# Kernel optimization log

Measured on AMD Instinct MI355X. Metric: run time of the kernel, lower is better.

The kernel has to match this reference:

```python
import jax, jax.numpy as jnp
import numpy as np

BN_EPS = 1e-5
LEAKY_SLOPE = 0.2

B, C, N, K, OUT = 8, 64, 4096, 32, 64


def setup_inputs() -> dict:
    key = jax.random.key(0)
    ks = jax.random.split(key, 8)
    return {
        "Graph_index": jax.random.randint(ks[0], (B, N, K), 0, N),
        "x": jax.random.normal(ks[1], (B, C, N), dtype=jnp.float32),
        "feature": jax.random.normal(ks[2], (B, OUT, N, K), dtype=jnp.float32),
        "W": jax.random.normal(ks[3], (OUT, 2 * C), dtype=jnp.float32) * 0.1,
        "gamma": jax.random.uniform(ks[4], (OUT,), dtype=jnp.float32) + 0.5,
        "beta": jax.random.normal(ks[5], (OUT,), dtype=jnp.float32) * 0.1,
        "bn_mean": jax.random.normal(ks[6], (OUT,), dtype=jnp.float32) * 0.1,
        "bn_var": jax.random.uniform(ks[7], (OUT,), dtype=jnp.float32) + 0.5,
    }


def reference(Graph_index, x, feature, W, gamma, beta, bn_mean, bn_var):
    b, c, n = x.shape
    k = Graph_index.shape[-1]
    # torch does x.view(B,N,C): a raw memory reinterpret, not a transpose
    xv = x.reshape(b, n, c)                                  # [B,N,C]
    feat = jnp.transpose(feature, (0, 2, 3, 1))              # [B,N,K,out]
    # index_points: gather K neighbors per point
    nb = jax.vmap(lambda xb, ib: xb[ib])(xv, Graph_index)    # [B,N,K,C]
    centre = xv[:, :, None, :]                               # [B,N,1,C]
    delta_f = jnp.concatenate([centre - nb, nb], axis=3)     # [B,N,K,2C]
    # 1x1 conv over channels == matmul
    e = jnp.einsum("bnkc,oc->bnko", delta_f, W)              # [B,N,K,out]
    # BatchNorm2d (eval-mode affine with running stats)
    inv = gamma * jax.lax.rsqrt(bn_var + BN_EPS)
    e = e * inv + (beta - bn_mean * inv)
    e = jnp.where(e >= 0, e, LEAKY_SLOPE * e)                # LeakyReLU(0.2)
    attention = jax.nn.softmax(e, axis=2)                    # softmax over K
    graph_feature = jnp.sum(attention * feat, axis=2)        # [B,N,out]
    return jnp.transpose(graph_feature, (0, 2, 1))           # [B,out,N]
```

## Files before the change

kernel.cpp:

```cpp
#include <hip/hip_runtime.h>


constexpr int B_ = 8, C_ = 64, N_ = 4096, K_ = 32, O_ = 64;
typedef float v4 __attribute__((ext_vector_type(4)));

__global__ __launch_bounds__(256) void gat_pre(
    const float* __restrict__ x, const float* __restrict__ W,
    const float* __restrict__ gamma, const float* __restrict__ beta,
    const float* __restrict__ bn_mean, const float* __restrict__ bn_var,
    float* __restrict__ T, float* __restrict__ U)
{
    __shared__ float xsT[64][68];
    __shared__ float wt1[64][68];
    __shared__ float wtd[64][68];

    const int blk = blockIdx.x;
    const int b = blk & 7;
    const int n_base = (blk >> 3) << 6;
    const int t = threadIdx.x;

    const float* xb = x + ((size_t)b * N_ + n_base) * C_;
    #pragma unroll
    for (int r = 0; r < 4; ++r) {
        const int e0 = r * 1024 + t * 4;
        const v4 v = __builtin_nontemporal_load(reinterpret_cast<const v4*>(xb + e0));
        xsT[(e0 + 0) & 63][(e0 + 0) >> 6] = v.x;
        xsT[(e0 + 1) & 63][(e0 + 1) >> 6] = v.y;
        xsT[(e0 + 2) & 63][(e0 + 2) >> 6] = v.z;
        xsT[(e0 + 3) & 63][(e0 + 3) >> 6] = v.w;
    }
    #pragma unroll
    for (int i = 0; i < 16; ++i) {
        const int idx = i * 256 + t;
        const int o = idx >> 6, c = idx & 63;
        const float w1 = W[o * 128 + c];
        const float w2 = W[o * 128 + 64 + c];
        wt1[c][o] = w1;
        wtd[c][o] = w2 - w1;
    }
    __syncthreads();

    const int o0 = (t & 15) * 4;
    const int n0 = (t >> 4) * 4;
    float accT[4][4] = {};
    float accU[4][4] = {};
    #pragma unroll 4
    for (int c = 0; c < 64; ++c) {
        const v4 xn = *reinterpret_cast<const v4*>(&xsT[c][n0]);
        const v4 w1 = *reinterpret_cast<const v4*>(&wt1[c][o0]);
        const v4 wd = *reinterpret_cast<const v4*>(&wtd[c][o0]);
        const float xa[4] = {xn.x, xn.y, xn.z, xn.w};
        const float wa[4] = {w1.x, w1.y, w1.z, w1.w};
        const float da[4] = {wd.x, wd.y, wd.z, wd.w};
        #pragma unroll
        for (int i = 0; i < 4; ++i)
            #pragma unroll
            for (int j = 0; j < 4; ++j) {
                accT[i][j] = fmaf(xa[i], wa[j], accT[i][j]);
                accU[i][j] = fmaf(xa[i], da[j], accU[i][j]);
            }
    }

    float inv[4], bias[4];
    #pragma unroll
    for (int j = 0; j < 4; ++j) {
        const int o = o0 + j;
        const float iv = gamma[o] * rsqrtf(bn_var[o] + 1e-5f);
        inv[j] = iv;
        bias[j] = beta[o] - bn_mean[o] * iv;
    }
    #pragma unroll
    for (int i = 0; i < 4; ++i) {
        const int n = n_base + n0 + i;
        float tvv[4], uvv[4];
        #pragma unroll
        for (int j = 0; j < 4; ++j) {
            tvv[j] = fmaf(accT[i][j], inv[j], bias[j]);
            uvv[j] = accU[i][j] * inv[j];
        }
        float* tp = T + ((size_t)b * N_ + n) * O_ + o0;
        float* up = U + ((size_t)b * N_ + n) * O_ + o0;
        *reinterpret_cast<v4*>(tp) = (v4){tvv[0], tvv[1], tvv[2], tvv[3]};
        *reinterpret_cast<v4*>(up) = (v4){uvv[0], uvv[1], uvv[2], uvv[3]};
    }
}

__global__ __launch_bounds__(256) void gat_main(
    const int* __restrict__ gi, const float* __restrict__ feat,
    const float* __restrict__ T, const float* __restrict__ U,
    float* __restrict__ out)
{
    __shared__ float tmp[64][17];
    const int blk = blockIdx.x;
    const int b = blk & 7;
    const int n_base = (blk >> 3) * 16;
    const int t = threadIdx.x;
    const int w = t >> 6;
    const int lane = t & 63;

    const float* Ub = U + (size_t)b * N_ * O_ + lane;

    #pragma unroll 1
    for (int r = 0; r < 4; ++r) {
        const int n = n_base + w * 4 + r;
        int vi = 0;
        if (lane < 32) vi = __builtin_nontemporal_load(&gi[((size_t)b * N_ + n) * K_ + lane]);
        const float tv = __builtin_nontemporal_load(&T[((size_t)b * N_ + n) * O_ + lane]);

        const v4* fp = reinterpret_cast<const v4*>(feat + (((size_t)b * O_ + lane) * N_ + n) * K_);
        v4 f[8];
        #pragma unroll
        for (int k4 = 0; k4 < 8; ++k4) f[k4] = fp[k4];

        float u[32];
        #pragma unroll
        for (int k = 0; k < 32; ++k) {
            const int m = __shfl(vi, k, 64);
            u[k] = Ub[(size_t)m * O_];
        }

        float emax = -3.0e38f;
        #pragma unroll
        for (int k = 0; k < 32; ++k) {
            float ev = tv + u[k];
            ev = fmaxf(ev, 0.2f * ev);
            u[k] = ev;
            emax = fmaxf(emax, ev);
        }

        float num = 0.f, den = 0.f;
        #pragma unroll
        for (int k4 = 0; k4 < 8; ++k4) {
            const float p0 = __expf(u[k4 * 4 + 0] - emax);
            const float p1 = __expf(u[k4 * 4 + 1] - emax);
            const float p2 = __expf(u[k4 * 4 + 2] - emax);
            const float p3 = __expf(u[k4 * 4 + 3] - emax);
            num = fmaf(p0, f[k4].x, num); den += p0;
            num = fmaf(p1, f[k4].y, num); den += p1;
            num = fmaf(p2, f[k4].z, num); den += p2;
            num = fmaf(p3, f[k4].w, num); den += p3;
        }
        tmp[lane][w * 4 + r] = num / den;
    }
    __syncthreads();

    #pragma unroll
    for (int r = 0; r < 4; ++r) {
        const int o = r * 16 + (t >> 4);
        const int ns = t & 15;
        __builtin_nontemporal_store(tmp[o][ns],
            &out[((size_t)b * O_ + o) * N_ + n_base + ns]);
    }
}

extern "C" void kernel_launch(void* const* d_in, const int* in_sizes, int n_in,
                              void* d_out, int out_size, void* d_ws, size_t ws_size,
                              hipStream_t stream) {
    const int*   gi      = (const int*)d_in[0];
    const float* x       = (const float*)d_in[1];
    const float* feat    = (const float*)d_in[2];
    const float* W       = (const float*)d_in[3];
    const float* gamma   = (const float*)d_in[4];
    const float* beta    = (const float*)d_in[5];
    const float* bn_mean = (const float*)d_in[6];
    const float* bn_var  = (const float*)d_in[7];
    float* out = (float*)d_out;

    float* T = (float*)d_ws;
    float* U = T + (size_t)B_ * N_ * O_;

    gat_pre<<<dim3(B_ * (N_ / 64)), dim3(256), 0, stream>>>(
        x, W, gamma, beta, bn_mean, bn_var, T, U);
    gat_main<<<dim3(B_ * (N_ / 16)), dim3(256), 0, stream>>>(
        gi, feat, T, U, out);
}
```

Measured before the change: 425.5 us.

## Stage feature tiles through swizzled LDS for coalesced global loads

The main kernel now loads the feature tensor cooperatively across the block so that each wavefront's loads cover 4 consecutive points' K values contiguously per channel, instead of each lane reading a strided 128-byte row. The data is staged in a 32KB XOR-swizzled shared buffer and then read per lane. Index and T loads for all four iterations are also hoisted ahead of the loop. This targets poor coalescing on the dominant feature stream, at the cost of extra LDS traffic, two block barriers per iteration, and lower occupancy from the larger shared allocation.

```diff
diff --git a/kernel.cpp b/kernel.cpp
--- a/kernel.cpp
+++ b/kernel.cpp
@@ -3,6 +3,7 @@
 
 constexpr int B_ = 8, C_ = 64, N_ = 4096, K_ = 32, O_ = 64;
 typedef float v4 __attribute__((ext_vector_type(4)));
+typedef float v2 __attribute__((ext_vector_type(2)));
 
 __global__ __launch_bounds__(256) void gat_pre(
     const float* __restrict__ x, const float* __restrict__ W,
@@ -90,7 +91,9 @@
     const float* __restrict__ T, const float* __restrict__ U,
     float* __restrict__ out)
 {
+    __shared__ float fs[4 * 2048];
     __shared__ float tmp[64][17];
+
     const int blk = blockIdx.x;
     const int b = blk & 7;
     const int n_base = (blk >> 3) * 16;
@@ -100,47 +103,70 @@
 
     const float* Ub = U + (size_t)b * N_ * O_ + lane;
 
+    int   vi[4];
+    float tv[4];
+    #pragma unroll
+    for (int s = 0; s < 4; ++s) {
+        const int n = n_base + s * 4 + w;
+        vi[s] = (lane < 32)
+            ? __builtin_nontemporal_load(&gi[((size_t)b * N_ + n) * K_ + lane]) : 0;
+        tv[s] = __builtin_nontemporal_load(&T[((size_t)b * N_ + n) * O_ + lane]);
+    }
+
+    const int swz = 2 * (lane & 15);
+
     #pragma unroll 1
-    for (int r = 0; r < 4; ++r) {
-        const int n = n_base + w * 4 + r;
-        int vi = 0;
-        if (lane < 32) vi = __builtin_nontemporal_load(&gi[((size_t)b * N_ + n) * K_ + lane]);
-        const float tv = __builtin_nontemporal_load(&T[((size_t)b * N_ + n) * O_ + lane]);
-
-        const v4* fp = reinterpret_cast<const v4*>(feat + (((size_t)b * O_ + lane) * N_ + n) * K_);
-        v4 f[8];
-        #pragma unroll
-        for (int k4 = 0; k4 < 8; ++k4) f[k4] = fp[k4];
-
+    for (int s = 0; s < 4; ++s) {
         float u[32];
         #pragma unroll
         for (int k = 0; k < 32; ++k) {
-            const int m = __shfl(vi, k, 64);
+            const int m = __shfl(vi[s], k, 64);
             u[k] = Ub[(size_t)m * O_];
         }
 
+        const float* fbase = feat + ((size_t)b * O_ * N_ + (size_t)(n_base + s * 4)) * K_;
+        v4 g[8];
+        #pragma unroll
+        for (int i = 0; i < 8; ++i) {
+            const int f4 = t + 256 * i;
+            const int o = f4 >> 5, j = f4 & 31;
+            g[i] = __builtin_nontemporal_load(
+                reinterpret_cast<const v4*>(fbase + (size_t)o * (N_ * K_) + j * 4));
+        }
+
+        __syncthreads();
+        #pragma unroll
+        for (int i = 0; i < 8; ++i) {
+            const int f4 = t + 256 * i;
+            const int o = f4 >> 5, j = f4 & 31;
+            const int nr = j >> 3, kk = (j * 4) & 31;
+            const int sw = 2 * (o & 15);
+            const int base = nr * 2048 + o * 32;
+            *reinterpret_cast<v2*>(&fs[base + ((kk + 0) ^ sw)]) = (v2){g[i].x, g[i].y};
+            *reinterpret_cast<v2*>(&fs[base + ((kk + 2) ^ sw)]) = (v2){g[i].z, g[i].w};
+        }
+        __syncthreads();
+
         float emax = -3.0e38f;
         #pragma unroll
         for (int k = 0; k < 32; ++k) {
-            float ev = tv + u[k];
+            float ev = tv[s] + u[k];
             ev = fmaxf(ev, 0.2f * ev);
             u[k] = ev;
             emax = fmaxf(emax, ev);
         }
 
+        const int rbase = w * 2048 + lane * 32;
         float num = 0.f, den = 0.f;
         #pragma unroll
-        for (int k4 = 0; k4 < 8; ++k4) {
-            const float p0 = __expf(u[k4 * 4 + 0] - emax);
-            const float p1 = __expf(u[k4 * 4 + 1] - emax);
-            const float p2 = __expf(u[k4 * 4 + 2] - emax);
-            const float p3 = __expf(u[k4 * 4 + 3] - emax);
-            num = fmaf(p0, f[k4].x, num); den += p0;
-            num = fmaf(p1, f[k4].y, num); den += p1;
-            num = fmaf(p2, f[k4].z, num); den += p2;
-            num = fmaf(p3, f[k4].w, num); den += p3;
-        }
-        tmp[lane][w * 4 + r] = num / den;
+        for (int k2 = 0; k2 < 16; ++k2) {
+            const v2 f = *reinterpret_cast<const v2*>(&fs[rbase + ((2 * k2) ^ swz)]);
+            const float p0 = __expf(u[k2 * 2 + 0] - emax);
+            const float p1 = __expf(u[k2 * 2 + 1] - emax);
+            num = fmaf(p0, f.x, num); den += p0;
+            num = fmaf(p1, f.y, num); den += p1;
+        }
+        tmp[lane][s * 4 + w] = num / den;
     }
     __syncthreads();
 
```

Result: faster. 378.8 us (-11.0%).
